# Kernel optimization log

Hardware: AMD Instinct MI355X
Metric: run time of the kernel (lower is better)

## Reference

```python
import jax, jax.numpy as jnp
import numpy as np

B, N, FD = 8, 32768, 32
NUM_GROUP, GROUP_SIZE = 1024, 32
RAD_FIVE_DEG = 0.087266  # radians_of_five_degrees threshold


def setup_inputs() -> dict:
    key = jax.random.key(0)
    k1, k2, k3 = jax.random.split(key, 3)
    coord = jax.random.normal(k1, (B * N, 3), dtype=jnp.float32)
    feat = jax.random.normal(k2, (B * N, FD), dtype=jnp.float32)
    labels = jax.random.randint(k3, (B * N,), 0, 20)
    offset = jnp.cumsum(jnp.full((B,), N, dtype=jnp.int32))  # [N, 2N, ..., BN]
    return {"coord": coord, "feat": feat, "labels": labels, "offset": offset}


def _fps(coords, num_samples):
    """Farthest point sampling on one cloud. coords: [N,3] -> [num_samples] indices."""
    d = jnp.sum((coords - coords[0]) ** 2, axis=-1)  # dist to first selected point

    def step(dist, _):
        idx = jnp.argmax(dist)
        nd = jnp.sum((coords - coords[idx]) ** 2, axis=-1)
        return jnp.minimum(dist, nd), idx

    _, idxs = jax.lax.scan(step, d, None, length=num_samples - 1)
    return jnp.concatenate([jnp.zeros((1,), dtype=idxs.dtype), idxs])


def reference(coord, feat, labels, offset):
    b = offset.shape[0]
    n = coord.shape[0] // b
    c = coord.reshape(b, n, 3)        # [B,N,3]
    f = feat.reshape(b, n, FD)        # [B,N,FD]
    lab = labels.reshape(b, n)

    # --- FPS: num_group samples per cloud ---
    s_idx = jax.vmap(_fps, in_axes=(0, None))(c, NUM_GROUP)  # [B,G]

    s_xyz = jnp.take_along_axis(c, s_idx[..., None], axis=1)          # [B,G,3]
    s_feat = jnp.take_along_axis(f, s_idx[..., None], axis=1)         # [B,G,FD]
    s_labels = jnp.take_along_axis(lab, s_idx, axis=1)                # [B,G]

    # --- kNN within each cloud: [B,G,N] distance matrix, top-k smallest ---
    d2 = jnp.sum((s_xyz[:, :, None, :] - c[:, None, :, :]) ** 2, axis=-1)  # [B,G,N]
    _, n_idx = jax.lax.top_k(-d2, GROUP_SIZE)                              # [B,G,K] ascending distance

    # gather neighbor features: [B,G,K,FD]
    s_n_feat = jax.vmap(lambda fb, ib: fb[ib])(f, n_idx)

    # --- point curvature: 2*atan2(||a*|b| - |a|*b||, ||a*|b| + |a|*b||) ---
    a = s_feat[:, :, None, :]                                   # [B,G,1,FD]
    an = jnp.linalg.norm(a, axis=-1, keepdims=True)             # [B,G,1,1]
    bn = jnp.linalg.norm(s_n_feat, axis=-1, keepdims=True)      # [B,G,K,1]
    num = jnp.linalg.norm(a * bn - an * s_n_feat, axis=-1)      # [B,G,K]
    den = jnp.linalg.norm(a * bn + an * s_n_feat, axis=-1)      # [B,G,K]
    angles = 2.0 * jnp.arctan2(num, den)                        # [B,G,K]
    # drop self neighbor (first, distance 0), mean over remaining
    p_curv = jnp.mean(angles[:, :, 1:], axis=-1, keepdims=True)  # [B,G,1]

    shape_weight = (p_curv > RAD_FIVE_DEG).astype(jnp.int32).squeeze(-1)  # [B,G]
    feat_out = jnp.concatenate([s_feat, p_curv], axis=-1)                 # [B,G,FD+1]

    # flat index back to parent (global flat indexing, per original flat layout)
    s_idx_flat = s_idx + jnp.arange(b, dtype=s_idx.dtype)[:, None] * n

    return (s_xyz.reshape(-1, 3),
            feat_out.reshape(-1, FD + 1),
            shape_weight.reshape(-1),
            s_labels.reshape(-1),
            s_idx_flat.reshape(-1))
```

## Files before the change

kernel.cpp:

```cpp
#include <hip/hip_runtime.h>
#include <math.h>

#define BATCH   8
#define NPTS    32768
#define FDIM    32
#define NGROUP  1024
#define GSIZE   32
#define KLANE   8

#define NBLK    8
#define FTPB    512
#define CHUNK   (NPTS / NBLK)
#define NFPSBLK (BATCH * NBLK)
#define KNNQPB  8
#define NKNNBLK ((BATCH * NGROUP) / KNNQPB)

__device__ __forceinline__ float dist2f(float ax, float ay, float az,
                                        float bx, float by, float bz) {
  float dx = __fsub_rn(ax, bx);
  float dy = __fsub_rn(ay, by);
  float dz = __fsub_rn(az, bz);
  return __fadd_rn(__fadd_rn(__fmul_rn(dx, dx), __fmul_rn(dy, dy)),
                   __fmul_rn(dz, dz));
}

#define X8(M) M(0) M(1) M(2) M(3) M(4) M(5) M(6) M(7)

__global__ __launch_bounds__(FTPB) void fused_kernel(
    const float* __restrict__ coord, const float* __restrict__ feat,
    const int* __restrict__ labels,
    unsigned long long* __restrict__ slots,
    int* __restrict__ s_idx_ws,
    float* __restrict__ out) {
  __shared__ float redv[8];
  __shared__ int   redp[8];
  __shared__ unsigned long long bcast;

  const int bx   = blockIdx.x;
  const int tid  = threadIdx.x;
  const int lane = tid & 63;
  const int wid  = tid >> 6;

  if (bx < NFPSBLK) {
    const int b    = bx & 7;
    const int bk   = bx >> 3;
    const float* __restrict__ c = coord + (size_t)b * NPTS * 3;
    const float3* __restrict__ c3 = (const float3*)c;
    const int pbase = bk * CHUNK + tid;

#define DECL8(i) float x##i, y##i, z##i, d##i;
    X8(DECL8)
#undef DECL8

    float qx = c[0], qy = c[1], qz = c[2];
    float bestv = -1.0f; int bestp = 0;
#define LOAD8(i) { int p = pbase + (i) * FTPB; float3 v = c3[p];            \
    x##i = v.x; y##i = v.y; z##i = v.z;                                      \
    float t2 = dist2f(v.x, v.y, v.z, qx, qy, qz); d##i = t2;                 \
    if (t2 > bestv) { bestv = t2; bestp = p; } }
    X8(LOAD8)
#undef LOAD8

    if (bk == 0 && tid == 0)
      __hip_atomic_store(&s_idx_ws[b * NGROUP + 0], 1, __ATOMIC_RELAXED,
                         __HIP_MEMORY_SCOPE_AGENT);

    for (int t = 1; t < NGROUP; ++t) {
      float v = bestv; int p = bestp;
      #pragma unroll
      for (int m = 1; m < 64; m <<= 1) {
        float ov = __shfl_xor(v, m, 64);
        int   op = __shfl_xor(p, m, 64);
        if (ov > v || (ov == v && op < p)) { v = ov; p = op; }
      }
      if (lane == 0) { redv[wid] = v; redp[wid] = p; }
      __syncthreads();

      if (wid == 0) {
        float gv = redv[lane & 7]; int gp = redp[lane & 7];
        #pragma unroll
        for (int m = 1; m < 8; m <<= 1) {
          float ov = __shfl_xor(gv, m, 64);
          int   op = __shfl_xor(gp, m, 64);
          if (ov > gv || (ov == gv && op < gp)) { gv = ov; gp = op; }
        }
        unsigned long long* base = slots + (size_t)(t & 1) * (BATCH * NBLK);
        if (lane == 0) {
          unsigned long long pk = ((unsigned long long)t << 47)
                                | ((unsigned long long)__float_as_uint(gv) << 15)
                                | (unsigned long long)(0x7FFF - gp);
          __hip_atomic_store(base + (b << 3) + bk, pk, __ATOMIC_RELEASE,
                             __HIP_MEMORY_SCOPE_AGENT);
        }
        unsigned long long pk2 = 0;
        if (lane < 8) {
          const unsigned long long* sl = base + (b << 3) + lane;
          do {
            pk2 = __hip_atomic_load(sl, __ATOMIC_ACQUIRE,
                                    __HIP_MEMORY_SCOPE_AGENT);
          } while ((int)(pk2 >> 47) != t);
        }
        #pragma unroll
        for (int m = 1; m < 8; m <<= 1) {
          unsigned long long o = __shfl_xor(pk2, m, 64);
          if (o > pk2) pk2 = o;
        }
        if (lane == 0) bcast = pk2;
      }
      __syncthreads();

      const unsigned long long wpk = bcast;
      const int gp = 0x7FFF - (int)(wpk & 0x7FFF);
      if (bk == 0 && tid == 0)
        __hip_atomic_store(&s_idx_ws[b * NGROUP + t], gp + 1,
                           __ATOMIC_RELAXED, __HIP_MEMORY_SCOPE_AGENT);
      if (t == NGROUP - 1) break;

      float3 q = c3[gp];
      qx = q.x; qy = q.y; qz = q.z;
      bestv = -1.0f; bestp = 0;
#define UPD8(i) { float t2 = dist2f(x##i, y##i, z##i, qx, qy, qz);           \
    float nd = fminf(d##i, t2); d##i = nd;                                   \
    if (nd > bestv) { bestv = nd; bestp = pbase + (i) * FTPB; } }
      X8(UPD8)
#undef UPD8
    }
    return;
  }

  const int qid = (bx - NFPSBLK) * KNNQPB + wid;
  const int b   = qid >> 10;
  const float* __restrict__ c = coord + (size_t)b * NPTS * 3;

  const int tq = qid & (NGROUP - 1);
  int enc = __hip_atomic_load(&s_idx_ws[qid], __ATOMIC_RELAXED,
                              __HIP_MEMORY_SCOPE_AGENT);
  for (int i = tq >> 2; i > 0 && enc == 0; --i) {
    __builtin_amdgcn_s_sleep(127);
    enc = __hip_atomic_load(&s_idx_ws[qid], __ATOMIC_RELAXED,
                            __HIP_MEMORY_SCOPE_AGENT);
  }
  while (enc == 0) {
    __builtin_amdgcn_s_sleep(64);
    enc = __hip_atomic_load(&s_idx_ws[qid], __ATOMIC_RELAXED,
                            __HIP_MEMORY_SCOPE_AGENT);
  }
  const int sp = __builtin_amdgcn_readfirstlane(enc - 1);
  const int gq = b * NPTS + sp;
  const float qx = coord[(size_t)gq * 3 + 0];
  const float qy = coord[(size_t)gq * 3 + 1];
  const float qz = coord[(size_t)gq * 3 + 2];

  float lv[KLANE]; int li[KLANE];
  #pragma unroll
  for (int j = 0; j < KLANE; ++j) { lv[j] = 1e30f; li[j] = 0x7fffffff; }

#define INSERT(D2, P) \
  if ((D2) < lv[KLANE - 1]) { \
    _Pragma("unroll") \
    for (int j = KLANE - 1; j >= 1; --j) { \
      bool up = (D2) < lv[j - 1]; \
      float nv = up ? lv[j - 1] : (((D2) < lv[j]) ? (D2) : lv[j]); \
      int   ni = up ? li[j - 1] : (((D2) < lv[j]) ? (P)  : li[j]); \
      lv[j] = nv; li[j] = ni; \
    } \
    if ((D2) < lv[0]) { lv[0] = (D2); li[0] = (P); } \
  }

  for (int s = 0; s < NPTS / 256; ++s) {
    int p = (s << 8) | (lane << 2);
    const float4* c4 = (const float4*)(c + (size_t)p * 3);
    float4 f0 = c4[0], f1 = c4[1], f2 = c4[2];
    float dA = dist2f(f0.x, f0.y, f0.z, qx, qy, qz);
    float dB = dist2f(f0.w, f1.x, f1.y, qx, qy, qz);
    float dC = dist2f(f1.z, f1.w, f2.x, qx, qy, qz);
    float dD = dist2f(f2.y, f2.z, f2.w, qx, qy, qz);
    INSERT(dA, p);
    INSERT(dB, p + 1);
    INSERT(dC, p + 2);
    INSERT(dD, p + 3);
  }
#undef INSERT

  int nbp = 0;
  for (int r = 0; r < GSIZE; ++r) {
    float mv = lv[0]; int mp = li[0];
    #pragma unroll
    for (int m = 1; m < 64; m <<= 1) {
      float ov = __shfl_xor(mv, m, 64);
      int   op = __shfl_xor(mp, m, 64);
      if (ov < mv || (ov == mv && op < mp)) { mv = ov; mp = op; }
    }
    if (lane == r) nbp = mp;
    if (lv[0] == mv && li[0] == mp) {
      #pragma unroll
      for (int j = 0; j < KLANE - 1; ++j) { lv[j] = lv[j + 1]; li[j] = li[j + 1]; }
      lv[KLANE - 1] = 1e30f; li[KLANE - 1] = 0x7fffffff;
    }
  }

  const float* aRow = feat + (size_t)gq * FDIM;
  float my_a = (lane < FDIM) ? aRow[lane] : 0.0f;

  float ang = 0.0f;
  if (lane >= 1 && lane < GSIZE) {
    const float4* a4 = (const float4*)aRow;
    const float4* b4 = (const float4*)(feat + ((size_t)b * NPTS + nbp) * FDIM);
    float4 av[FDIM / 4], bv[FDIM / 4];
    float aa = 0.0f, bb = 0.0f;
    #pragma unroll
    for (int k = 0; k < FDIM / 4; ++k) {
      av[k] = a4[k]; bv[k] = b4[k];
      aa += av[k].x * av[k].x + av[k].y * av[k].y + av[k].z * av[k].z + av[k].w * av[k].w;
      bb += bv[k].x * bv[k].x + bv[k].y * bv[k].y + bv[k].z * bv[k].z + bv[k].w * bv[k].w;
    }
    float an = sqrtf(aa), bn = sqrtf(bb);
    float num2 = 0.0f, den2 = 0.0f;
    #pragma unroll
    for (int k = 0; k < FDIM / 4; ++k) {
      float n0 = av[k].x * bn - an * bv[k].x, dd0 = av[k].x * bn + an * bv[k].x;
      float n1 = av[k].y * bn - an * bv[k].y, dd1 = av[k].y * bn + an * bv[k].y;
      float n2 = av[k].z * bn - an * bv[k].z, dd2 = av[k].z * bn + an * bv[k].z;
      float n3 = av[k].w * bn - an * bv[k].w, dd3 = av[k].w * bn + an * bv[k].w;
      num2 += n0 * n0 + n1 * n1 + n2 * n2 + n3 * n3;
      den2 += dd0 * dd0 + dd1 * dd1 + dd2 * dd2 + dd3 * dd3;
    }
    ang = 2.0f * atan2f(sqrtf(num2), sqrtf(den2));
  }

  float tot = ang;
  #pragma unroll
  for (int m = 1; m < 64; m <<= 1) tot += __shfl_xor(tot, m, 64);
  float p_curv = tot / 31.0f;

  float* out_xyz  = out;
  float* out_feat = out + (size_t)BATCH * NGROUP * 3;
  float* out_sw   = out_feat + (size_t)BATCH * NGROUP * (FDIM + 1);
  float* out_lab  = out_sw  + (size_t)BATCH * NGROUP;
  float* out_sif  = out_lab + (size_t)BATCH * NGROUP;

  if (lane < FDIM)  out_feat[(size_t)qid * (FDIM + 1) + lane] = my_a;
  if (lane == FDIM) out_feat[(size_t)qid * (FDIM + 1) + FDIM] = p_curv;
  if (lane == 0) {
    out_xyz[(size_t)qid * 3 + 0] = qx;
    out_xyz[(size_t)qid * 3 + 1] = qy;
    out_xyz[(size_t)qid * 3 + 2] = qz;
    out_sw[qid]  = (p_curv > 0.087266f) ? 1.0f : 0.0f;
    out_lab[qid] = (float)labels[gq];
    out_sif[qid] = (float)gq;
  }
}

extern "C" void kernel_launch(void* const* d_in, const int* in_sizes, int n_in,
                              void* d_out, int out_size, void* d_ws, size_t ws_size,
                              hipStream_t stream) {
  const float* coord  = (const float*)d_in[0];
  const float* feat   = (const float*)d_in[1];
  const int*   labels = (const int*)d_in[2];

  unsigned long long* slots = (unsigned long long*)d_ws;
  int* s_idx_ws = (int*)((char*)d_ws +
                         2 * BATCH * NBLK * sizeof(unsigned long long));
  const size_t zbytes = 2 * BATCH * NBLK * sizeof(unsigned long long)
                      + (size_t)BATCH * NGROUP * sizeof(int);

  hipMemsetAsync(d_ws, 0, zbytes, stream);
  fused_kernel<<<NFPSBLK + NKNNBLK, FTPB, 0, stream>>>(
      coord, feat, labels, slots, s_idx_ws, (float*)d_out);
}
```

Measured before the change: 2.895 ms.

## Exchange winner coordinates in FPS slots and poll per-wave without block barrier

Each FPS block now picks the winning point's xyz from its registers and packs distance, index and coordinates into three 64-bit slots, so the next query point needs no dependent global load of coord. All waves poll the 24 slots directly with a ballot instead of wave 0 polling and broadcasting through shared memory, which removes one __syncthreads per FPS iteration. The cost is three times as many atomic stores and loads per step, relaxed ordering, and more bit-packing work.

```diff
diff --git a/kernel.cpp b/kernel.cpp
--- a/kernel.cpp
+++ b/kernel.cpp
@@ -14,6 +14,8 @@
 #define NFPSBLK (BATCH * NBLK)
 #define KNNQPB  8
 #define NKNNBLK ((BATCH * NGROUP) / KNNQPB)
+
+typedef unsigned long long u64;
 
 __device__ __forceinline__ float dist2f(float ax, float ay, float az,
                                         float bx, float by, float bz) {
@@ -29,12 +31,12 @@
 __global__ __launch_bounds__(FTPB) void fused_kernel(
     const float* __restrict__ coord, const float* __restrict__ feat,
     const int* __restrict__ labels,
-    unsigned long long* __restrict__ slots,
+    u64* __restrict__ slots,
     int* __restrict__ s_idx_ws,
     float* __restrict__ out) {
   __shared__ float redv[8];
   __shared__ int   redp[8];
-  __shared__ unsigned long long bcast;
+  __shared__ float redx[8], redy[8], redz[8];
 
   const int bx   = blockIdx.x;
   const int tid  = threadIdx.x;
@@ -73,51 +75,86 @@
         int   op = __shfl_xor(p, m, 64);
         if (ov > v || (ov == v && op < p)) { v = ov; p = op; }
       }
-      if (lane == 0) { redv[wid] = v; redp[wid] = p; }
+      {
+        int rel = p - bk * CHUNK;
+        int ol  = rel & 63;
+        int ii  = rel >> 9;
+        float sx = 0.f, sy = 0.f, sz = 0.f;
+#define SEL(i) if (ii == (i)) { sx = x##i; sy = y##i; sz = z##i; }
+        X8(SEL)
+#undef SEL
+        sx = __shfl(sx, ol, 64); sy = __shfl(sy, ol, 64);
+        sz = __shfl(sz, ol, 64);
+        if (lane == 0) {
+          redv[wid] = v; redp[wid] = p;
+          redx[wid] = sx; redy[wid] = sy; redz[wid] = sz;
+        }
+      }
       __syncthreads();
 
+      u64* base = slots + ((size_t)(t & 1) * BATCH + b) * 24;
       if (wid == 0) {
-        float gv = redv[lane & 7]; int gp = redp[lane & 7];
+        int widx = lane & 7;
+        float gvv = redv[widx]; int gpp = redp[widx]; int gw = widx;
         #pragma unroll
         for (int m = 1; m < 8; m <<= 1) {
-          float ov = __shfl_xor(gv, m, 64);
-          int   op = __shfl_xor(gp, m, 64);
-          if (ov > gv || (ov == gv && op < gp)) { gv = ov; gp = op; }
+          float ov = __shfl_xor(gvv, m, 64);
+          int   op = __shfl_xor(gpp, m, 64);
+          int   ow = __shfl_xor(gw, m, 64);
+          if (ov > gvv || (ov == gvv && op < gpp)) { gvv = ov; gpp = op; gw = ow; }
         }
-        unsigned long long* base = slots + (size_t)(t & 1) * (BATCH * NBLK);
         if (lane == 0) {
-          unsigned long long pk = ((unsigned long long)t << 47)
-                                | ((unsigned long long)__float_as_uint(gv) << 15)
-                                | (unsigned long long)(0x7FFF - gp);
-          __hip_atomic_store(base + (b << 3) + bk, pk, __ATOMIC_RELEASE,
+          unsigned int xb = __float_as_uint(redx[gw]);
+          unsigned int yb = __float_as_uint(redy[gw]);
+          unsigned int zb = __float_as_uint(redz[gw]);
+          unsigned int db = __float_as_uint(gvv);
+          u64 S0 = ((u64)t << 54) | ((u64)db << 22)
+                 | ((u64)(0x7FFF - gpp) << 7) | (u64)(xb >> 25);
+          u64 S1 = ((u64)t << 54) | ((u64)(xb & 0x1FFFFFFu) << 29)
+                 | (u64)(yb >> 3);
+          u64 S2 = ((u64)t << 54) | ((u64)(yb & 7u) << 32) | (u64)zb;
+          __hip_atomic_store(base + bk,      S0, __ATOMIC_RELAXED,
+                             __HIP_MEMORY_SCOPE_AGENT);
+          __hip_atomic_store(base + 8 + bk,  S1, __ATOMIC_RELAXED,
+                             __HIP_MEMORY_SCOPE_AGENT);
+          __hip_atomic_store(base + 16 + bk, S2, __ATOMIC_RELAXED,
                              __HIP_MEMORY_SCOPE_AGENT);
         }
-        unsigned long long pk2 = 0;
-        if (lane < 8) {
-          const unsigned long long* sl = base + (b << 3) + lane;
-          do {
-            pk2 = __hip_atomic_load(sl, __ATOMIC_ACQUIRE,
-                                    __HIP_MEMORY_SCOPE_AGENT);
-          } while ((int)(pk2 >> 47) != t);
-        }
-        #pragma unroll
-        for (int m = 1; m < 8; m <<= 1) {
-          unsigned long long o = __shfl_xor(pk2, m, 64);
-          if (o > pk2) pk2 = o;
-        }
-        if (lane == 0) bcast = pk2;
       }
-      __syncthreads();
-
-      const unsigned long long wpk = bcast;
-      const int gp = 0x7FFF - (int)(wpk & 0x7FFF);
-      if (bk == 0 && tid == 0)
+
+      const int pl = (lane < 24) ? lane : 0;
+      u64 pk2; bool ok;
+      do {
+        pk2 = __hip_atomic_load(base + pl, __ATOMIC_RELAXED,
+                                __HIP_MEMORY_SCOPE_AGENT);
+        ok = (lane >= 24) || ((int)(pk2 >> 54) == t);
+      } while (__ballot(ok) != ~0ULL);
+
+      u64 s0 = __shfl(pk2, lane & 7, 64);
+      int wbk = lane & 7;
+      #pragma unroll
+      for (int m = 1; m < 8; m <<= 1) {
+        u64 o  = __shfl_xor(s0, m, 64);
+        int ob = __shfl_xor(wbk, m, 64);
+        if (o > s0) { s0 = o; wbk = ob; }
+      }
+      const int gp = 0x7FFF - (int)((s0 >> 7) & 0x7FFF);
+      u64 S1w = __shfl(pk2, 8 + wbk, 64);
+      u64 S2w = __shfl(pk2, 16 + wbk, 64);
+      unsigned int xb = (unsigned int)(((s0 & 0x7Fu) << 25)
+                       | ((S1w >> 29) & 0x1FFFFFFu));
+      unsigned int yb = (unsigned int)(((S1w & 0x1FFFFFFFu) << 3)
+                       | ((S2w >> 32) & 0x7u));
+      unsigned int zb = (unsigned int)(S2w & 0xFFFFFFFFu);
+
+      if (bk == 0 && wid == 0 && lane == 0)
         __hip_atomic_store(&s_idx_ws[b * NGROUP + t], gp + 1,
                            __ATOMIC_RELAXED, __HIP_MEMORY_SCOPE_AGENT);
       if (t == NGROUP - 1) break;
 
-      float3 q = c3[gp];
-      qx = q.x; qy = q.y; qz = q.z;
+      qx = __uint_as_float(xb);
+      qy = __uint_as_float(yb);
+      qz = __uint_as_float(zb);
       bestv = -1.0f; bestp = 0;
 #define UPD8(i) { float t2 = dist2f(x##i, y##i, z##i, qx, qy, qz);           \
     float nd = fminf(d##i, t2); d##i = nd;                                   \
@@ -258,10 +295,9 @@
   const float* feat   = (const float*)d_in[1];
   const int*   labels = (const int*)d_in[2];
 
-  unsigned long long* slots = (unsigned long long*)d_ws;
-  int* s_idx_ws = (int*)((char*)d_ws +
-                         2 * BATCH * NBLK * sizeof(unsigned long long));
-  const size_t zbytes = 2 * BATCH * NBLK * sizeof(unsigned long long)
+  u64* slots = (u64*)d_ws;
+  int* s_idx_ws = (int*)((char*)d_ws + 2 * BATCH * 24 * sizeof(u64));
+  const size_t zbytes = 2 * BATCH * 24 * sizeof(u64)
                       + (size_t)BATCH * NGROUP * sizeof(int);
 
   hipMemsetAsync(d_ws, 0, zbytes, stream);
```

Measured after the change: 4.348 ms. 1.5x slower.
